# Kernel tuning notes

Hardware: AMD Instinct MI355X
Metric: run time of the kernel (lower is better)

The kernel has to match this reference:

```python
import jax, jax.numpy as jnp
import numpy as np

B, H, W = 16, 64, 64
MODES = 16          # fno_modes (undefined constant in source; standard choice)
HID = 12            # FNO hidden_channels
LIFT = 256          # neuralop default lifting/projection channel width
OUT_CH = 640
N_LAYERS = 4
EPS = 1e-5


def setup_inputs() -> dict:
    key = jax.random.key(0)
    ks = iter(jax.random.split(key, 40))
    r = lambda shape, s=0.05: jax.random.normal(next(ks), shape, dtype=jnp.float32) * s
    inp = {
        "x": jax.random.normal(next(ks), (B, 1, H, W), dtype=jnp.float32),
        "condition": jax.random.normal(next(ks), (B, 2), dtype=jnp.float32),
        # BatchNorm affine params
        "bn2_g": jnp.ones((1,), jnp.float32), "bn2_b": jnp.zeros((1,), jnp.float32),
        "bn1_g": jnp.ones((2,), jnp.float32), "bn1_b": jnp.zeros((2,), jnp.float32),
        # Branch_net: 2 -> 50 -> 50 -> 1, tanh after each
        "b_w1": r((2, 50), 0.5), "b_b1": jnp.zeros((50,), jnp.float32),
        "b_w2": r((50, 50), 0.2), "b_b2": jnp.zeros((50,), jnp.float32),
        "b_w3": r((50, 1), 0.2), "b_b3": jnp.zeros((1,), jnp.float32),
        # FNO lifting MLP: 1 -> 256 -> 12 (1x1 convs)
        "l1_w": r((1, LIFT), 0.5), "l1_b": jnp.zeros((LIFT,), jnp.float32),
        "l2_w": r((LIFT, HID), 0.1), "l2_b": jnp.zeros((HID,), jnp.float32),
        # Spectral conv complex weights (stored real/imag), per layer:
        # block1 = low positive freqs, block2 = negative freqs along axis -2
        "sw1r": r((N_LAYERS, HID, HID, MODES, MODES)),
        "sw1i": r((N_LAYERS, HID, HID, MODES, MODES)),
        "sw2r": r((N_LAYERS, HID, HID, MODES, MODES)),
        "sw2i": r((N_LAYERS, HID, HID, MODES, MODES)),
        # per-layer linear (1x1 conv) skip
        "sk_w": r((N_LAYERS, HID, HID), 0.2),
        "sk_b": jnp.zeros((N_LAYERS, HID), jnp.float32),
        # projection MLP: 12 -> 256 -> 640
        "p1_w": r((HID, LIFT), 0.2), "p1_b": jnp.zeros((LIFT,), jnp.float32),
        "p2_w": r((LIFT, OUT_CH), 0.1), "p2_b": jnp.zeros((OUT_CH,), jnp.float32),
    }
    return inp


def _forward(x, condition, bn2_g, bn2_b, bn1_g, bn1_b,
             b_w1, b_b1, b_w2, b_b2, b_w3, b_b3,
             l1_w, l1_b, l2_w, l2_b,
             sw1r, sw1i, sw2r, sw2i, sk_w, sk_b,
             p1_w, p1_b, p2_w, p2_b):
    gelu = lambda v: jax.nn.gelu(v, approximate=False)

    # BatchNorm2d(1), training-mode batch stats over (B, H, W)
    m = jnp.mean(x, axis=(0, 2, 3), keepdims=True)
    v = jnp.var(x, axis=(0, 2, 3), keepdims=True)
    x_n = (x - m) * jax.lax.rsqrt(v + EPS) * bn2_g[None, :, None, None] + bn2_b[None, :, None, None]

    # BatchNorm1d(2) over batch
    cm = jnp.mean(condition, axis=0, keepdims=True)
    cv = jnp.var(condition, axis=0, keepdims=True)
    c_n = (condition - cm) * jax.lax.rsqrt(cv + EPS) * bn1_g + bn1_b

    # Branch MLP with tanh activations -> [B, 1]
    h = jnp.tanh(c_n @ b_w1 + b_b1)
    h = jnp.tanh(h @ b_w2 + b_b2)
    branch = jnp.tanh(h @ b_w3 + b_b3)

    # FNO lifting: 1x1 conv MLP  [B,1,H,W] -> [B,HID,H,W]
    t = gelu(jnp.einsum('bchw,cd->bdhw', x_n, l1_w) + l1_b[None, :, None, None])
    t = jnp.einsum('bdhw,de->behw', t, l2_w) + l2_b[None, :, None, None]

    Mo = MODES
    for i in range(N_LAYERS):
        xft = jnp.fft.rfft2(t)                          # [B,HID,H,W//2+1] complex
        w1 = sw1r[i] + 1j * sw1i[i]
        w2 = sw2r[i] + 1j * sw2i[i]
        top = jnp.einsum('bchw,cohw->bohw', xft[:, :, :Mo, :Mo], w1)
        bot = jnp.einsum('bchw,cohw->bohw', xft[:, :, -Mo:, :Mo], w2)
        out_ft = jnp.zeros((B, HID, H, W // 2 + 1), dtype=xft.dtype)
        out_ft = out_ft.at[:, :, :Mo, :Mo].set(top).at[:, :, -Mo:, :Mo].set(bot)
        spec = jnp.fft.irfft2(out_ft, s=(H, W))
        skip = jnp.einsum('bchw,co->bohw', t, sk_w[i]) + sk_b[i][None, :, None, None]
        t = spec + skip
        if i < N_LAYERS - 1:
            t = gelu(t)

    # projection: [B,HID,H,W] -> [B,640,H,W]
    q = gelu(jnp.einsum('bchw,cd->bdhw', t, p1_w) + p1_b[None, :, None, None])
    fno_out = jnp.einsum('bdhw,de->behw', q, p2_w) + p2_b[None, :, None, None]

    final = fno_out * branch[:, :, None, None]          # broadcast [B,1,1,1]
    return jnp.transpose(final, (0, 2, 1, 3))           # [B, H, 640, W]


def reference(x, condition, bn2_g, bn2_b, bn1_g, bn1_b,
              b_w1, b_b1, b_w2, b_b2, b_w3, b_b3,
              l1_w, l1_b, l2_w, l2_b,
              sw1r, sw1i, sw2r, sw2i, sk_w, sk_b,
              p1_w, p1_b, p2_w, p2_b):
    return _forward(x, condition, bn2_g, bn2_b, bn1_g, bn1_b,
                    b_w1, b_b1, b_w2, b_b2, b_w3, b_b3,
                    l1_w, l1_b, l2_w, l2_b,
                    sw1r, sw1i, sw2r, sw2i, sk_w, sk_b,
                    p1_w, p1_b, p2_w, p2_b)
```

## Files before the change

### kernel.cpp

```cpp
#include <hip/hip_runtime.h>
#include <math.h>

#define BB 16
#define PIX 4096
#define NPIX 65536
#define HID 12
#define LIFT 256
#define OUT_CH 640
#define EPS 1e-5f

typedef _Float16 half8 __attribute__((ext_vector_type(8)));
typedef float floatx16 __attribute__((ext_vector_type(16)));

__device__ __forceinline__ float gelu_f(float x) {
    return 0.5f * x * (1.0f + erff(x * 0.70710678118654752f));
}

__global__ __launch_bounds__(256) void k_bn_stats(const float* __restrict__ x,
                                                  float* __restrict__ stats) {
    __shared__ float s1[256], s2[256];
    float a = 0.f, b = 0.f;
    for (int i = threadIdx.x; i < NPIX; i += 256) { float v = x[i]; a += v; b += v * v; }
    s1[threadIdx.x] = a; s2[threadIdx.x] = b;
    __syncthreads();
    for (int off = 128; off > 0; off >>= 1) {
        if (threadIdx.x < off) { s1[threadIdx.x] += s1[threadIdx.x + off];
                                 s2[threadIdx.x] += s2[threadIdx.x + off]; }
        __syncthreads();
    }
    if (threadIdx.x == 0) {
        float m = s1[0] / (float)NPIX;
        float var = s2[0] / (float)NPIX - m * m;
        stats[0] = m;
        stats[1] = rsqrtf(var + EPS);
    }
}

__global__ __launch_bounds__(64) void k_branch(const float* __restrict__ cond,
                                               const float* __restrict__ g1, const float* __restrict__ b1,
                                               const float* __restrict__ w1, const float* __restrict__ bb1,
                                               const float* __restrict__ w2, const float* __restrict__ bb2,
                                               const float* __restrict__ w3, const float* __restrict__ bb3,
                                               float* __restrict__ br_out) {
    __shared__ float cm[2], cistd[2];
    int t = threadIdx.x;
    if (t < 2) {
        float s = 0.f;
        for (int i = 0; i < 16; i++) s += cond[i * 2 + t];
        float m = s / 16.f;
        float v = 0.f;
        for (int i = 0; i < 16; i++) { float d = cond[i * 2 + t] - m; v += d * d; }
        v /= 16.f;
        cm[t] = m; cistd[t] = rsqrtf(v + EPS);
    }
    __syncthreads();
    if (t < 16) {
        float c0 = (cond[t * 2 + 0] - cm[0]) * cistd[0] * g1[0] + b1[0];
        float c1 = (cond[t * 2 + 1] - cm[1]) * cistd[1] * g1[1] + b1[1];
        float h1[50], h2[50];
        for (int j = 0; j < 50; j++) h1[j] = tanhf(bb1[j] + c0 * w1[j] + c1 * w1[50 + j]);
        for (int j = 0; j < 50; j++) {
            float acc = bb2[j];
            for (int k = 0; k < 50; k++) acc += h1[k] * w2[k * 50 + j];
            h2[j] = tanhf(acc);
        }
        float acc = bb3[0];
        for (int k = 0; k < 50; k++) acc += h2[k] * w3[k];
        br_out[t] = tanhf(acc);
    }
}

__global__ __launch_bounds__(256) void k_lift(const float* __restrict__ x, const float* __restrict__ stats,
                                              const float* __restrict__ g2, const float* __restrict__ b2,
                                              const float* __restrict__ l1w, const float* __restrict__ l1b,
                                              const float* __restrict__ l2w, const float* __restrict__ l2b,
                                              float* __restrict__ t0) {
    int p = blockIdx.x * 256 + threadIdx.x;
    float m = stats[0], istd = stats[1];
    float xn = (x[p] - m) * istd * g2[0] + b2[0];
    float acc[HID];
#pragma unroll
    for (int e = 0; e < HID; e++) acc[e] = l2b[e];
    for (int d = 0; d < LIFT; d++) {
        float g = gelu_f(xn * l1w[d] + l1b[d]);
#pragma unroll
        for (int e = 0; e < HID; e++) acc[e] += g * l2w[d * HID + e];
    }
    int b = p >> 12, px = p & 4095;
#pragma unroll
    for (int e = 0; e < HID; e++) t0[(b * HID + e) * PIX + px] = acc[e];
}

__global__ __launch_bounds__(256) void k_fwd_w(const float* __restrict__ tin, float2* __restrict__ A) {
    __shared__ float tl[64 * 65];
    __shared__ float ct[64], st[64];
    int bc = blockIdx.x;
    int tid = threadIdx.x;
    if (tid < 64) { float s, c; sincospif(tid * (1.0f / 32.0f), &s, &c); ct[tid] = c; st[tid] = s; }
    const float* src = tin + bc * PIX;
    for (int i = tid; i < PIX; i += 256) {
        int h = i >> 6, w = i & 63;
        tl[h * 65 + w] = src[i];
    }
    __syncthreads();
    for (int o = tid; o < 1024; o += 256) {
        int kw = o >> 6, h = o & 63;
        float xr = 0.f, xi = 0.f;
        for (int w = 0; w < 64; w++) {
            int j = (kw * w) & 63;
            float v = tl[h * 65 + w];
            xr += v * ct[j];
            xi -= v * st[j];
        }
        A[(bc * 16 + kw) * 64 + h] = make_float2(xr, xi);
    }
}

__global__ __launch_bounds__(384) void k_fwd_h_mul(const float2* __restrict__ A,
                                                   const float* __restrict__ w1r, const float* __restrict__ w1i,
                                                   const float* __restrict__ w2r, const float* __restrict__ w2i,
                                                   float2* __restrict__ O) {
    __shared__ float2 Al[12 * 64];
    __shared__ float2 Xl[12 * 32];
    __shared__ float ct[64], st[64];
    int b = blockIdx.x >> 4;
    int kw = blockIdx.x & 15;
    int tid = threadIdx.x;
    if (tid < 64) { float s, c; sincospif(tid * (1.0f / 32.0f), &s, &c); ct[tid] = c; st[tid] = s; }
    for (int i = tid; i < 12 * 64; i += 384) {
        int c = i >> 6, h = i & 63;
        Al[i] = A[((b * 12 + c) * 16 + kw) * 64 + h];
    }
    __syncthreads();
    {
        int c = tid >> 5, kh = tid & 31;
        int f = (kh < 16) ? kh : kh + 32;
        float xr = 0.f, xi = 0.f;
        for (int h = 0; h < 64; h++) {
            int j = (f * h) & 63;
            float2 a = Al[c * 64 + h];
            float cc = ct[j], ss = st[j];
            xr += a.x * cc + a.y * ss;
            xi += a.y * cc - a.x * ss;
        }
        Xl[c * 32 + kh] = make_float2(xr, xi);
    }
    __syncthreads();
    {
        int o = tid >> 5, kh = tid & 31;
        int khr = kh & 15;
        const float* wr = (kh < 16) ? w1r : w2r;
        const float* wi = (kh < 16) ? w1i : w2i;
        float orr = 0.f, oii = 0.f;
        for (int c = 0; c < 12; c++) {
            float2 xv = Xl[c * 32 + kh];
            int wIdx = ((c * 12 + o) * 16 + khr) * 16 + kw;
            float wrv = wr[wIdx], wiv = wi[wIdx];
            orr += xv.x * wrv - xv.y * wiv;
            oii += xv.x * wiv + xv.y * wrv;
        }
        O[((b * 12 + o) * 32 + kh) * 16 + kw] = make_float2(orr, oii);
    }
}

__global__ __launch_bounds__(256) void k_inv(const float2* __restrict__ O, float* __restrict__ spec) {
    __shared__ float2 Ol[32 * 16];
    __shared__ float2 Yl[64 * 17];
    __shared__ float ct[64], st[64];
    int bo = blockIdx.x;
    int tid = threadIdx.x;
    if (tid < 64) { float s, c; sincospif(tid * (1.0f / 32.0f), &s, &c); ct[tid] = c; st[tid] = s; }
    for (int i = tid; i < 512; i += 256) Ol[i] = O[bo * 512 + i];
    __syncthreads();
    for (int oidx = tid; oidx < 1024; oidx += 256) {
        int kw = oidx >> 6, h = oidx & 63;
        float yr = 0.f, yi = 0.f;
        for (int kh = 0; kh < 32; kh++) {
            int f = (kh < 16) ? kh : kh + 32;
            int j = (f * h) & 63;
            float2 ov = Ol[kh * 16 + kw];
            float cc = ct[j], ss = st[j];
            yr += ov.x * cc - ov.y * ss;
            yi += ov.x * ss + ov.y * cc;
        }
        Yl[h * 17 + kw] = make_float2(yr * (1.0f / 4096.0f), yi * (1.0f / 4096.0f));
    }
    __syncthreads();
    for (int i = tid; i < PIX; i += 256) {
        int h = i >> 6, w = i & 63;
        float acc = 0.f;
#pragma unroll
        for (int kw = 0; kw < 16; kw++) {
            int j = (kw * w) & 63;
            float2 yv = Yl[h * 17 + kw];
            float term = yv.x * ct[j] - yv.y * st[j];
            acc += (kw == 0) ? term : 2.0f * term;
        }
        spec[bo * PIX + i] = acc;
    }
}

__global__ __launch_bounds__(256) void k_skip(const float* __restrict__ tin, const float* __restrict__ spec,
                                              const float* __restrict__ skw, const float* __restrict__ skb,
                                              float* __restrict__ tout, int apply_gelu) {
    int p = blockIdx.x * 256 + threadIdx.x;
    int b = p >> 12, px = p & 4095;
    float tr[12];
#pragma unroll
    for (int c = 0; c < 12; c++) tr[c] = tin[(b * 12 + c) * PIX + px];
#pragma unroll
    for (int o = 0; o < 12; o++) {
        float v = spec[(b * 12 + o) * PIX + px] + skb[o];
#pragma unroll
        for (int c = 0; c < 12; c++) v += tr[c] * skw[c * 12 + o];
        if (apply_gelu) v = gelu_f(v);
        tout[(b * 12 + o) * PIX + px] = v;
    }
}

__global__ __launch_bounds__(256) void k_wt(const float* __restrict__ p2w, _Float16* __restrict__ wt) {
    int eg = blockIdx.x;
    int tid = threadIdx.x;
    for (int idx = tid; idx < 1024; idx += 256) {
        int m = idx & 31, kh = (idx >> 5) & 1, ks = idx >> 6;
        half8 v;
#pragma unroll
        for (int j = 0; j < 8; j++)
            v[j] = (_Float16)p2w[(ks * 16 + kh * 8 + j) * 640 + eg * 32 + m];
        *(half8*)&wt[eg * 8192 + ks * 512 + kh * 256 + m * 8] = v;
    }
}

__global__ __launch_bounds__(256, 2) void k_proj_mfma(const float* __restrict__ t,
                                                      const float* __restrict__ p1w,
                                                      const float* __restrict__ p1b,
                                                      const _Float16* __restrict__ wt,
                                                      const float* __restrict__ p2b,
                                                      const float* __restrict__ brn,
                                                      float* __restrict__ out) {
    __shared__ __align__(16) _Float16 ql[128 * 256];
    int pxb = blockIdx.x * 128;
    int eb  = blockIdx.y * 128;
    int tid = threadIdx.x;

    {
        int pxl = tid & 127;
        int dg  = tid >> 7;
        int px  = pxb + pxl;
        int b = px >> 12, pimg = px & 4095;
        float tv[12];
#pragma unroll
        for (int c = 0; c < 12; c++) tv[c] = t[(b * 12 + c) * PIX + pimg];
        int pg = pxl >> 5, pm = pxl & 31;
        for (int dd = 0; dd < 128; dd += 8) {
            half8 hv;
#pragma unroll
            for (int i = 0; i < 8; i++) {
                int d = dg * 128 + dd + i;
                float a = p1b[d];
#pragma unroll
                for (int c = 0; c < 12; c++) a += tv[c] * p1w[c * 256 + d];
                hv[i] = (_Float16)gelu_f(a);
            }
            int d0 = dg * 128 + dd;
            int ks = d0 >> 4, kh = (d0 >> 3) & 1;
            *(half8*)&ql[pg * 8192 + ks * 512 + kh * 256 + pm * 8] = hv;
        }
    }
    __syncthreads();

    int wave = tid >> 6, lane = tid & 63;
    int we = wave >> 1, wp = wave & 1;
    int lo = (lane >> 5) * 256 + (lane & 31) * 8;
    int eg0 = (eb + we * 64) >> 5;
    int pg0 = wp * 2;

    floatx16 acc[2][2];
#pragma unroll
    for (int a = 0; a < 2; a++)
#pragma unroll
        for (int b2 = 0; b2 < 2; b2++)
#pragma unroll
            for (int i = 0; i < 16; i++) acc[a][b2][i] = 0.f;

#pragma unroll
    for (int ks = 0; ks < 16; ks++) {
        half8 a0 = *(const half8*)(wt + eg0 * 8192 + ks * 512 + lo);
        half8 a1 = *(const half8*)(wt + (eg0 + 1) * 8192 + ks * 512 + lo);
        half8 b0 = *(const half8*)&ql[pg0 * 8192 + ks * 512 + lo];
        half8 b1 = *(const half8*)&ql[(pg0 + 1) * 8192 + ks * 512 + lo];
        acc[0][0] = __builtin_amdgcn_mfma_f32_32x32x16_f16(a0, b0, acc[0][0], 0, 0, 0);
        acc[0][1] = __builtin_amdgcn_mfma_f32_32x32x16_f16(a0, b1, acc[0][1], 0, 0, 0);
        acc[1][0] = __builtin_amdgcn_mfma_f32_32x32x16_f16(a1, b0, acc[1][0], 0, 0, 0);
        acc[1][1] = __builtin_amdgcn_mfma_f32_32x32x16_f16(a1, b1, acc[1][1], 0, 0, 0);
    }

    float brv = brn[pxb >> 12];
#pragma unroll
    for (int ta = 0; ta < 2; ta++) {
#pragma unroll
        for (int tb = 0; tb < 2; tb++) {
            int e_base = eb + we * 64 + ta * 32;
            int px = pxb + wp * 64 + tb * 32 + (lane & 31);
            int bh = px >> 6, w = px & 63;
            float* op = out + bh * 640 * 64 + w;
#pragma unroll
            for (int r = 0; r < 16; r++) {
                int row = (r & 3) + 8 * (r >> 2) + 4 * (lane >> 5);
                int e = e_base + row;
                op[e * 64] = (acc[ta][tb][r] + p2b[e]) * brv;
            }
        }
    }
}

extern "C" void kernel_launch(void* const* d_in, const int* in_sizes, int n_in,
                              void* d_out, int out_size, void* d_ws, size_t ws_size,
                              hipStream_t stream) {
    const float* x     = (const float*)d_in[0];
    const float* cond  = (const float*)d_in[1];
    const float* bn2_g = (const float*)d_in[2];
    const float* bn2_b = (const float*)d_in[3];
    const float* bn1_g = (const float*)d_in[4];
    const float* bn1_b = (const float*)d_in[5];
    const float* b_w1  = (const float*)d_in[6];
    const float* b_b1  = (const float*)d_in[7];
    const float* b_w2  = (const float*)d_in[8];
    const float* b_b2  = (const float*)d_in[9];
    const float* b_w3  = (const float*)d_in[10];
    const float* b_b3  = (const float*)d_in[11];
    const float* l1w   = (const float*)d_in[12];
    const float* l1b   = (const float*)d_in[13];
    const float* l2w   = (const float*)d_in[14];
    const float* l2b   = (const float*)d_in[15];
    const float* sw1r  = (const float*)d_in[16];
    const float* sw1i  = (const float*)d_in[17];
    const float* sw2r  = (const float*)d_in[18];
    const float* sw2i  = (const float*)d_in[19];
    const float* skw   = (const float*)d_in[20];
    const float* skb   = (const float*)d_in[21];
    const float* p1w   = (const float*)d_in[22];
    const float* p1b   = (const float*)d_in[23];
    const float* p2w   = (const float*)d_in[24];
    const float* p2b   = (const float*)d_in[25];

    float* ws = (float*)d_ws;
    float* stats = ws;
    float* brn   = ws + 2;
    float* t0    = ws + 32;
    float* t1    = t0 + 786432;
    float2* A    = (float2*)(t1 + 786432);
    float2* O    = A + 196608;
    float* spec  = (float*)(O + 98304);
    _Float16* wt = (_Float16*)(spec + 786432);

    k_bn_stats<<<1, 256, 0, stream>>>(x, stats);
    k_branch<<<1, 64, 0, stream>>>(cond, bn1_g, bn1_b, b_w1, b_b1, b_w2, b_b2, b_w3, b_b3, brn);
    k_lift<<<256, 256, 0, stream>>>(x, stats, bn2_g, bn2_b, l1w, l1b, l2w, l2b, t0);
    k_wt<<<20, 256, 0, stream>>>(p2w, wt);

    float* tin = t0;
    float* tout = t1;
    for (int l = 0; l < 4; l++) {
        k_fwd_w<<<192, 256, 0, stream>>>(tin, A);
        k_fwd_h_mul<<<256, 384, 0, stream>>>(A, sw1r + l * 36864, sw1i + l * 36864,
                                             sw2r + l * 36864, sw2i + l * 36864, O);
        k_inv<<<192, 256, 0, stream>>>(O, spec);
        k_skip<<<256, 256, 0, stream>>>(tin, spec, skw + l * 144, skb + l * 12, tout,
                                        (l < 3) ? 1 : 0);
        float* tmp = tin; tin = tout; tout = tmp;
    }

    k_proj_mfma<<<dim3(512, 5), 256, 0, stream>>>(tin, p1w, p1b, wt, p2b, brn, (float*)d_out);
}
```

Measured before the change: 810.9 us.

## Fuse pre-projection stages into one persistent kernel with grid barriers

```diff
diff --git a/kernel.cpp b/kernel.cpp
--- a/kernel.cpp
+++ b/kernel.cpp
@@ -1,13 +1,10 @@
 #include <hip/hip_runtime.h>
 #include <math.h>
 
-#define BB 16
 #define PIX 4096
 #define NPIX 65536
-#define HID 12
-#define LIFT 256
-#define OUT_CH 640
 #define EPS 1e-5f
+#define NBLK 256u
 
 typedef _Float16 half8 __attribute__((ext_vector_type(8)));
 typedef float floatx16 __attribute__((ext_vector_type(16)));
@@ -16,99 +13,41 @@
     return 0.5f * x * (1.0f + erff(x * 0.70710678118654752f));
 }
 
-__global__ __launch_bounds__(256) void k_bn_stats(const float* __restrict__ x,
-                                                  float* __restrict__ stats) {
-    __shared__ float s1[256], s2[256];
-    float a = 0.f, b = 0.f;
-    for (int i = threadIdx.x; i < NPIX; i += 256) { float v = x[i]; a += v; b += v * v; }
-    s1[threadIdx.x] = a; s2[threadIdx.x] = b;
+__device__ __forceinline__ void gbar(unsigned* cnt) {
+    __threadfence();
     __syncthreads();
-    for (int off = 128; off > 0; off >>= 1) {
-        if (threadIdx.x < off) { s1[threadIdx.x] += s1[threadIdx.x + off];
-                                 s2[threadIdx.x] += s2[threadIdx.x + off]; }
-        __syncthreads();
-    }
     if (threadIdx.x == 0) {
-        float m = s1[0] / (float)NPIX;
-        float var = s2[0] / (float)NPIX - m * m;
-        stats[0] = m;
-        stats[1] = rsqrtf(var + EPS);
-    }
-}
-
-__global__ __launch_bounds__(64) void k_branch(const float* __restrict__ cond,
-                                               const float* __restrict__ g1, const float* __restrict__ b1,
-                                               const float* __restrict__ w1, const float* __restrict__ bb1,
-                                               const float* __restrict__ w2, const float* __restrict__ bb2,
-                                               const float* __restrict__ w3, const float* __restrict__ bb3,
-                                               float* __restrict__ br_out) {
-    __shared__ float cm[2], cistd[2];
-    int t = threadIdx.x;
-    if (t < 2) {
-        float s = 0.f;
-        for (int i = 0; i < 16; i++) s += cond[i * 2 + t];
-        float m = s / 16.f;
-        float v = 0.f;
-        for (int i = 0; i < 16; i++) { float d = cond[i * 2 + t] - m; v += d * d; }
-        v /= 16.f;
-        cm[t] = m; cistd[t] = rsqrtf(v + EPS);
+        __hip_atomic_fetch_add(cnt, 1u, __ATOMIC_ACQ_REL, __HIP_MEMORY_SCOPE_AGENT);
+        while (__hip_atomic_load(cnt, __ATOMIC_ACQUIRE, __HIP_MEMORY_SCOPE_AGENT) < NBLK) {
+            __builtin_amdgcn_s_sleep(1);
+        }
     }
     __syncthreads();
-    if (t < 16) {
-        float c0 = (cond[t * 2 + 0] - cm[0]) * cistd[0] * g1[0] + b1[0];
-        float c1 = (cond[t * 2 + 1] - cm[1]) * cistd[1] * g1[1] + b1[1];
-        float h1[50], h2[50];
-        for (int j = 0; j < 50; j++) h1[j] = tanhf(bb1[j] + c0 * w1[j] + c1 * w1[50 + j]);
-        for (int j = 0; j < 50; j++) {
-            float acc = bb2[j];
-            for (int k = 0; k < 50; k++) acc += h1[k] * w2[k * 50 + j];
-            h2[j] = tanhf(acc);
-        }
-        float acc = bb3[0];
-        for (int k = 0; k < 50; k++) acc += h2[k] * w3[k];
-        br_out[t] = tanhf(acc);
-    }
-}
-
-__global__ __launch_bounds__(256) void k_lift(const float* __restrict__ x, const float* __restrict__ stats,
-                                              const float* __restrict__ g2, const float* __restrict__ b2,
-                                              const float* __restrict__ l1w, const float* __restrict__ l1b,
-                                              const float* __restrict__ l2w, const float* __restrict__ l2b,
-                                              float* __restrict__ t0) {
-    int p = blockIdx.x * 256 + threadIdx.x;
-    float m = stats[0], istd = stats[1];
-    float xn = (x[p] - m) * istd * g2[0] + b2[0];
-    float acc[HID];
-#pragma unroll
-    for (int e = 0; e < HID; e++) acc[e] = l2b[e];
-    for (int d = 0; d < LIFT; d++) {
-        float g = gelu_f(xn * l1w[d] + l1b[d]);
-#pragma unroll
-        for (int e = 0; e < HID; e++) acc[e] += g * l2w[d * HID + e];
-    }
-    int b = p >> 12, px = p & 4095;
-#pragma unroll
-    for (int e = 0; e < HID; e++) t0[(b * HID + e) * PIX + px] = acc[e];
-}
-
-__global__ __launch_bounds__(256) void k_fwd_w(const float* __restrict__ tin, float2* __restrict__ A) {
-    __shared__ float tl[64 * 65];
-    __shared__ float ct[64], st[64];
-    int bc = blockIdx.x;
-    int tid = threadIdx.x;
-    if (tid < 64) { float s, c; sincospif(tid * (1.0f / 32.0f), &s, &c); ct[tid] = c; st[tid] = s; }
-    const float* src = tin + bc * PIX;
-    for (int i = tid; i < PIX; i += 256) {
-        int h = i >> 6, w = i & 63;
-        tl[h * 65 + w] = src[i];
-    }
-    __syncthreads();
+    __threadfence();
+}
+
+struct FusedArgs {
+    const float *x, *cond;
+    const float *bn2_g, *bn2_b, *bn1_g, *bn1_b;
+    const float *b_w1, *b_b1, *b_w2, *b_b2, *b_w3, *b_b3;
+    const float *l1w, *l1b, *l2w, *l2b;
+    const float *sw1r, *sw1i, *sw2r, *sw2i, *skw, *skb;
+    const float *p2w;
+    unsigned *bar;
+    float *brn, *t0, *t1;
+    float2 *A, *O;
+    float *spec;
+    _Float16 *wt;
+};
+
+__device__ __forceinline__ void fwd_w_tile(const float* s_tl, const float* ct, const float* st,
+                                           int bc, float2* A, int tid) {
     for (int o = tid; o < 1024; o += 256) {
         int kw = o >> 6, h = o & 63;
         float xr = 0.f, xi = 0.f;
         for (int w = 0; w < 64; w++) {
             int j = (kw * w) & 63;
-            float v = tl[h * 65 + w];
+            float v = s_tl[h * 65 + w];
             xr += v * ct[j];
             xi -= v * st[j];
         }
@@ -116,131 +55,221 @@
     }
 }
 
-__global__ __launch_bounds__(384) void k_fwd_h_mul(const float2* __restrict__ A,
-                                                   const float* __restrict__ w1r, const float* __restrict__ w1i,
-                                                   const float* __restrict__ w2r, const float* __restrict__ w2i,
-                                                   float2* __restrict__ O) {
-    __shared__ float2 Al[12 * 64];
-    __shared__ float2 Xl[12 * 32];
+__global__ __launch_bounds__(256) void k_fused(FusedArgs a) {
+    __shared__ float s_tl[64 * 65];
+    __shared__ float s_aux[3200];
     __shared__ float ct[64], st[64];
-    int b = blockIdx.x >> 4;
-    int kw = blockIdx.x & 15;
-    int tid = threadIdx.x;
+    __shared__ float s_red[512];
+    __shared__ float cms[4];
+    int blk = blockIdx.x, tid = threadIdx.x;
+    int bi = 0;
+
     if (tid < 64) { float s, c; sincospif(tid * (1.0f / 32.0f), &s, &c); ct[tid] = c; st[tid] = s; }
-    for (int i = tid; i < 12 * 64; i += 384) {
-        int c = i >> 6, h = i & 63;
-        Al[i] = A[((b * 12 + c) * 16 + kw) * 64 + h];
-    }
-    __syncthreads();
+
+    float bn_m, bn_istd;
     {
-        int c = tid >> 5, kh = tid & 31;
-        int f = (kh < 16) ? kh : kh + 32;
-        float xr = 0.f, xi = 0.f;
-        for (int h = 0; h < 64; h++) {
-            int j = (f * h) & 63;
-            float2 a = Al[c * 64 + h];
-            float cc = ct[j], ss = st[j];
-            xr += a.x * cc + a.y * ss;
-            xi += a.y * cc - a.x * ss;
-        }
-        Xl[c * 32 + kh] = make_float2(xr, xi);
-    }
-    __syncthreads();
+        float aa = 0.f, bb = 0.f;
+        for (int i = tid; i < NPIX; i += 256) { float v = a.x[i]; aa += v; bb += v * v; }
+        s_red[tid] = aa; s_red[256 + tid] = bb;
+        __syncthreads();
+        for (int off = 128; off > 0; off >>= 1) {
+            if (tid < off) { s_red[tid] += s_red[tid + off]; s_red[256 + tid] += s_red[256 + tid + off]; }
+            __syncthreads();
+        }
+        bn_m = s_red[0] * (1.0f / NPIX);
+        float var = s_red[256] * (1.0f / NPIX) - bn_m * bn_m;
+        bn_istd = rsqrtf(var + EPS);
+    }
+
+    if (blk < 20) {
+        int eg = blk;
+        for (int idx = tid; idx < 1024; idx += 256) {
+            int m = idx & 31, kh = (idx >> 5) & 1, ks = idx >> 6;
+            half8 v;
+#pragma unroll
+            for (int j = 0; j < 8; j++)
+                v[j] = (_Float16)a.p2w[(ks * 16 + kh * 8 + j) * 640 + eg * 32 + m];
+            *(half8*)&a.wt[eg * 8192 + ks * 512 + kh * 256 + m * 8] = v;
+        }
+    }
+
+    if (blk == 255) {
+        if (tid < 2) {
+            float s = 0.f;
+            for (int i = 0; i < 16; i++) s += a.cond[i * 2 + tid];
+            float m = s / 16.f, v = 0.f;
+            for (int i = 0; i < 16; i++) { float d = a.cond[i * 2 + tid] - m; v += d * d; }
+            cms[tid] = m; cms[2 + tid] = rsqrtf(v / 16.f + EPS);
+        }
+        __syncthreads();
+        if (tid < 16) {
+            float c0 = (a.cond[tid * 2 + 0] - cms[0]) * cms[2] * a.bn1_g[0] + a.bn1_b[0];
+            float c1 = (a.cond[tid * 2 + 1] - cms[1]) * cms[3] * a.bn1_g[1] + a.bn1_b[1];
+            float h1[50], h2[50];
+            for (int j = 0; j < 50; j++) h1[j] = tanhf(a.b_b1[j] + c0 * a.b_w1[j] + c1 * a.b_w1[50 + j]);
+            for (int j = 0; j < 50; j++) {
+                float acc = a.b_b2[j];
+                for (int k = 0; k < 50; k++) acc += h1[k] * a.b_w2[k * 50 + j];
+                h2[j] = tanhf(acc);
+            }
+            float acc = a.b_b3[0];
+            for (int k = 0; k < 50; k++) acc += h2[k] * a.b_w3[k];
+            a.brn[tid] = tanhf(acc);
+        }
+    }
+
     {
-        int o = tid >> 5, kh = tid & 31;
-        int khr = kh & 15;
-        const float* wr = (kh < 16) ? w1r : w2r;
-        const float* wi = (kh < 16) ? w1i : w2i;
-        float orr = 0.f, oii = 0.f;
-        for (int c = 0; c < 12; c++) {
-            float2 xv = Xl[c * 32 + kh];
-            int wIdx = ((c * 12 + o) * 16 + khr) * 16 + kw;
-            float wrv = wr[wIdx], wiv = wi[wIdx];
-            orr += xv.x * wrv - xv.y * wiv;
-            oii += xv.x * wiv + xv.y * wrv;
-        }
-        O[((b * 12 + o) * 32 + kh) * 16 + kw] = make_float2(orr, oii);
-    }
-}
-
-__global__ __launch_bounds__(256) void k_inv(const float2* __restrict__ O, float* __restrict__ spec) {
-    __shared__ float2 Ol[32 * 16];
-    __shared__ float2 Yl[64 * 17];
-    __shared__ float ct[64], st[64];
-    int bo = blockIdx.x;
-    int tid = threadIdx.x;
-    if (tid < 64) { float s, c; sincospif(tid * (1.0f / 32.0f), &s, &c); ct[tid] = c; st[tid] = s; }
-    for (int i = tid; i < 512; i += 256) Ol[i] = O[bo * 512 + i];
-    __syncthreads();
-    for (int oidx = tid; oidx < 1024; oidx += 256) {
-        int kw = oidx >> 6, h = oidx & 63;
-        float yr = 0.f, yi = 0.f;
-        for (int kh = 0; kh < 32; kh++) {
-            int f = (kh < 16) ? kh : kh + 32;
-            int j = (f * h) & 63;
-            float2 ov = Ol[kh * 16 + kw];
-            float cc = ct[j], ss = st[j];
-            yr += ov.x * cc - ov.y * ss;
-            yi += ov.x * ss + ov.y * cc;
-        }
-        Yl[h * 17 + kw] = make_float2(yr * (1.0f / 4096.0f), yi * (1.0f / 4096.0f));
-    }
-    __syncthreads();
-    for (int i = tid; i < PIX; i += 256) {
-        int h = i >> 6, w = i & 63;
-        float acc = 0.f;
-#pragma unroll
-        for (int kw = 0; kw < 16; kw++) {
-            int j = (kw * w) & 63;
-            float2 yv = Yl[h * 17 + kw];
-            float term = yv.x * ct[j] - yv.y * st[j];
-            acc += (kw == 0) ? term : 2.0f * term;
-        }
-        spec[bo * PIX + i] = acc;
-    }
-}
-
-__global__ __launch_bounds__(256) void k_skip(const float* __restrict__ tin, const float* __restrict__ spec,
-                                              const float* __restrict__ skw, const float* __restrict__ skb,
-                                              float* __restrict__ tout, int apply_gelu) {
-    int p = blockIdx.x * 256 + threadIdx.x;
-    int b = p >> 12, px = p & 4095;
-    float tr[12];
-#pragma unroll
-    for (int c = 0; c < 12; c++) tr[c] = tin[(b * 12 + c) * PIX + px];
-#pragma unroll
-    for (int o = 0; o < 12; o++) {
-        float v = spec[(b * 12 + o) * PIX + px] + skb[o];
-#pragma unroll
-        for (int c = 0; c < 12; c++) v += tr[c] * skw[c * 12 + o];
-        if (apply_gelu) v = gelu_f(v);
-        tout[(b * 12 + o) * PIX + px] = v;
-    }
-}
-
-__global__ __launch_bounds__(256) void k_wt(const float* __restrict__ p2w, _Float16* __restrict__ wt) {
-    int eg = blockIdx.x;
-    int tid = threadIdx.x;
-    for (int idx = tid; idx < 1024; idx += 256) {
-        int m = idx & 31, kh = (idx >> 5) & 1, ks = idx >> 6;
-        half8 v;
-#pragma unroll
-        for (int j = 0; j < 8; j++)
-            v[j] = (_Float16)p2w[(ks * 16 + kh * 8 + j) * 640 + eg * 32 + m];
-        *(half8*)&wt[eg * 8192 + ks * 512 + kh * 256 + m * 8] = v;
-    }
-}
-
-__global__ __launch_bounds__(256, 2) void k_proj_mfma(const float* __restrict__ t,
-                                                      const float* __restrict__ p1w,
-                                                      const float* __restrict__ p1b,
-                                                      const _Float16* __restrict__ wt,
-                                                      const float* __restrict__ p2b,
-                                                      const float* __restrict__ brn,
-                                                      float* __restrict__ out) {
+        int p = blk * 256 + tid;
+        float xn = (a.x[p] - bn_m) * bn_istd * a.bn2_g[0] + a.bn2_b[0];
+        float acc[12];
+#pragma unroll
+        for (int e = 0; e < 12; e++) acc[e] = a.l2b[e];
+        for (int d = 0; d < 256; d++) {
+            float g = gelu_f(xn * a.l1w[d] + a.l1b[d]);
+#pragma unroll
+            for (int e = 0; e < 12; e++) acc[e] += g * a.l2w[d * 12 + e];
+        }
+        int b = p >> 12, px = p & 4095;
+#pragma unroll
+        for (int e = 0; e < 12; e++) a.t0[(b * 12 + e) * PIX + px] = acc[e];
+    }
+    gbar(&a.bar[bi++]);
+
+    const float* tin = a.t0;
+    float* tout = a.t1;
+
+    if (blk < 192) {
+        for (int i = tid; i < PIX; i += 256) s_tl[(i >> 6) * 65 + (i & 63)] = tin[blk * PIX + i];
+        __syncthreads();
+        fwd_w_tile(s_tl, ct, st, blk, a.A, tid);
+    }
+    gbar(&a.bar[bi++]);
+
+    for (int l = 0; l < 4; l++) {
+        const float* w1r = a.sw1r + l * 36864; const float* w1i = a.sw1i + l * 36864;
+        const float* w2r = a.sw2r + l * 36864; const float* w2i = a.sw2i + l * 36864;
+
+        {
+            int b = blk >> 4, kw = blk & 15;
+            float2* Al = (float2*)s_aux;
+            float2* Xl = (float2*)(s_aux + 1536);
+            for (int i = tid; i < 768; i += 256) {
+                int c = i >> 6, h = i & 63;
+                Al[i] = a.A[((b * 12 + c) * 16 + kw) * 64 + h];
+            }
+            __syncthreads();
+            for (int o = tid; o < 384; o += 256) {
+                int c = o >> 5, kh = o & 31;
+                int f = (kh < 16) ? kh : kh + 32;
+                float xr = 0.f, xi = 0.f;
+                for (int h = 0; h < 64; h++) {
+                    int j = (f * h) & 63;
+                    float2 av = Al[c * 64 + h];
+                    float cc = ct[j], ss = st[j];
+                    xr += av.x * cc + av.y * ss;
+                    xi += av.y * cc - av.x * ss;
+                }
+                Xl[c * 32 + kh] = make_float2(xr, xi);
+            }
+            __syncthreads();
+            for (int o2 = tid; o2 < 384; o2 += 256) {
+                int o = o2 >> 5, kh = o2 & 31;
+                int khr = kh & 15;
+                const float* wr = (kh < 16) ? w1r : w2r;
+                const float* wi = (kh < 16) ? w1i : w2i;
+                float orr = 0.f, oii = 0.f;
+                for (int c = 0; c < 12; c++) {
+                    float2 xv = Xl[c * 32 + kh];
+                    int wIdx = ((c * 12 + o) * 16 + khr) * 16 + kw;
+                    float wrv = wr[wIdx], wiv = wi[wIdx];
+                    orr += xv.x * wrv - xv.y * wiv;
+                    oii += xv.x * wiv + xv.y * wrv;
+                }
+                a.O[((b * 12 + o) * 32 + kh) * 16 + kw] = make_float2(orr, oii);
+            }
+        }
+        gbar(&a.bar[bi++]);
+
+        if (blk < 192) {
+            int b = blk / 12, oc = blk % 12;
+            float2* Ol = (float2*)s_aux;
+            float2* Yl = (float2*)(s_aux + 1024);
+            for (int i = tid; i < 512; i += 256) Ol[i] = a.O[blk * 512 + i];
+            __syncthreads();
+            for (int oidx = tid; oidx < 1024; oidx += 256) {
+                int kw = oidx >> 6, h = oidx & 63;
+                float yr = 0.f, yi = 0.f;
+                for (int kh = 0; kh < 32; kh++) {
+                    int f = (kh < 16) ? kh : kh + 32;
+                    int j = (f * h) & 63;
+                    float2 ov = Ol[kh * 16 + kw];
+                    float cc = ct[j], ss = st[j];
+                    yr += ov.x * cc - ov.y * ss;
+                    yi += ov.x * ss + ov.y * cc;
+                }
+                Yl[h * 17 + kw] = make_float2(yr * (1.0f / 4096.0f), yi * (1.0f / 4096.0f));
+            }
+            __syncthreads();
+            for (int i = tid; i < PIX; i += 256) {
+                int h = i >> 6, w = i & 63;
+                float acc = 0.f;
+#pragma unroll
+                for (int kw = 0; kw < 16; kw++) {
+                    int j = (kw * w) & 63;
+                    float2 yv = Yl[h * 17 + kw];
+                    float term = yv.x * ct[j] - yv.y * st[j];
+                    acc += (kw == 0) ? term : 2.0f * term;
+                }
+                s_tl[h * 65 + w] = acc;
+            }
+            __syncthreads();
+            if (l < 3) {
+                for (int i = tid; i < PIX; i += 256) {
+                    int h = i >> 6, w = i & 63;
+                    float v = s_tl[h * 65 + w] + a.skb[l * 12 + oc];
+                    for (int c = 0; c < 12; c++)
+                        v += tin[(b * 12 + c) * PIX + i] * a.skw[l * 144 + c * 12 + oc];
+                    v = gelu_f(v);
+                    s_tl[h * 65 + w] = v;
+                    tout[(b * 12 + oc) * PIX + i] = v;
+                }
+                __syncthreads();
+                fwd_w_tile(s_tl, ct, st, blk, a.A, tid);
+            } else {
+                for (int i = tid; i < PIX; i += 256)
+                    a.spec[blk * PIX + i] = s_tl[(i >> 6) * 65 + (i & 63)];
+            }
+        }
+        gbar(&a.bar[bi++]);
+
+        if (l < 3) { const float* tmp = tin; tin = tout; tout = (float*)tmp; }
+    }
+
+    {
+        int p = blk * 256 + tid;
+        int b = p >> 12, px = p & 4095;
+        float tr[12];
+#pragma unroll
+        for (int c = 0; c < 12; c++) tr[c] = tin[(b * 12 + c) * PIX + px];
+#pragma unroll
+        for (int o = 0; o < 12; o++) {
+            float v = a.spec[(b * 12 + o) * PIX + px] + a.skb[36 + o];
+#pragma unroll
+            for (int c = 0; c < 12; c++) v += tr[c] * a.skw[432 + c * 12 + o];
+            tout[(b * 12 + o) * PIX + px] = v;
+        }
+    }
+}
+
+__global__ __launch_bounds__(256, 2) void k_proj2(const float* __restrict__ t,
+                                                  const float* __restrict__ p1w,
+                                                  const float* __restrict__ p1b,
+                                                  const _Float16* __restrict__ wt,
+                                                  const float* __restrict__ p2b,
+                                                  const float* __restrict__ brn,
+                                                  float* __restrict__ out) {
     __shared__ __align__(16) _Float16 ql[128 * 256];
     int pxb = blockIdx.x * 128;
-    int eb  = blockIdx.y * 128;
     int tid = threadIdx.x;
 
     {
@@ -257,10 +286,10 @@
 #pragma unroll
             for (int i = 0; i < 8; i++) {
                 int d = dg * 128 + dd + i;
-                float a = p1b[d];
-#pragma unroll
-                for (int c = 0; c < 12; c++) a += tv[c] * p1w[c * 256 + d];
-                hv[i] = (_Float16)gelu_f(a);
+                float aa = p1b[d];
+#pragma unroll
+                for (int c = 0; c < 12; c++) aa += tv[c] * p1w[c * 256 + d];
+                hv[i] = (_Float16)gelu_f(aa);
             }
             int d0 = dg * 128 + dd;
             int ks = d0 >> 4, kh = (d0 >> 3) & 1;
@@ -272,43 +301,47 @@
     int wave = tid >> 6, lane = tid & 63;
     int we = wave >> 1, wp = wave & 1;
     int lo = (lane >> 5) * 256 + (lane & 31) * 8;
-    int eg0 = (eb + we * 64) >> 5;
     int pg0 = wp * 2;
-
-    floatx16 acc[2][2];
-#pragma unroll
-    for (int a = 0; a < 2; a++)
-#pragma unroll
-        for (int b2 = 0; b2 < 2; b2++)
-#pragma unroll
-            for (int i = 0; i < 16; i++) acc[a][b2][i] = 0.f;
-
-#pragma unroll
-    for (int ks = 0; ks < 16; ks++) {
-        half8 a0 = *(const half8*)(wt + eg0 * 8192 + ks * 512 + lo);
-        half8 a1 = *(const half8*)(wt + (eg0 + 1) * 8192 + ks * 512 + lo);
-        half8 b0 = *(const half8*)&ql[pg0 * 8192 + ks * 512 + lo];
-        half8 b1 = *(const half8*)&ql[(pg0 + 1) * 8192 + ks * 512 + lo];
-        acc[0][0] = __builtin_amdgcn_mfma_f32_32x32x16_f16(a0, b0, acc[0][0], 0, 0, 0);
-        acc[0][1] = __builtin_amdgcn_mfma_f32_32x32x16_f16(a0, b1, acc[0][1], 0, 0, 0);
-        acc[1][0] = __builtin_amdgcn_mfma_f32_32x32x16_f16(a1, b0, acc[1][0], 0, 0, 0);
-        acc[1][1] = __builtin_amdgcn_mfma_f32_32x32x16_f16(a1, b1, acc[1][1], 0, 0, 0);
-    }
-
     float brv = brn[pxb >> 12];
-#pragma unroll
-    for (int ta = 0; ta < 2; ta++) {
-#pragma unroll
-        for (int tb = 0; tb < 2; tb++) {
-            int e_base = eb + we * 64 + ta * 32;
-            int px = pxb + wp * 64 + tb * 32 + (lane & 31);
-            int bh = px >> 6, w = px & 63;
-            float* op = out + bh * 640 * 64 + w;
-#pragma unroll
-            for (int r = 0; r < 16; r++) {
-                int row = (r & 3) + 8 * (r >> 2) + 4 * (lane >> 5);
-                int e = e_base + row;
-                op[e * 64] = (acc[ta][tb][r] + p2b[e]) * brv;
+
+    for (int ebi = 0; ebi < 5; ebi++) {
+        int eb = ebi * 128;
+        int eg0 = (eb + we * 64) >> 5;
+
+        floatx16 acc[2][2];
+#pragma unroll
+        for (int aa = 0; aa < 2; aa++)
+#pragma unroll
+            for (int b2 = 0; b2 < 2; b2++)
+#pragma unroll
+                for (int i = 0; i < 16; i++) acc[aa][b2][i] = 0.f;
+
+#pragma unroll
+        for (int ks = 0; ks < 16; ks++) {
+            half8 a0 = *(const half8*)(wt + eg0 * 8192 + ks * 512 + lo);
+            half8 a1 = *(const half8*)(wt + (eg0 + 1) * 8192 + ks * 512 + lo);
+            half8 b0 = *(const half8*)&ql[pg0 * 8192 + ks * 512 + lo];
+            half8 b1 = *(const half8*)&ql[(pg0 + 1) * 8192 + ks * 512 + lo];
+            acc[0][0] = __builtin_amdgcn_mfma_f32_32x32x16_f16(a0, b0, acc[0][0], 0, 0, 0);
+            acc[0][1] = __builtin_amdgcn_mfma_f32_32x32x16_f16(a0, b1, acc[0][1], 0, 0, 0);
+            acc[1][0] = __builtin_amdgcn_mfma_f32_32x32x16_f16(a1, b0, acc[1][0], 0, 0, 0);
+            acc[1][1] = __builtin_amdgcn_mfma_f32_32x32x16_f16(a1, b1, acc[1][1], 0, 0, 0);
+        }
+
+#pragma unroll
+        for (int ta = 0; ta < 2; ta++) {
+#pragma unroll
+            for (int tb = 0; tb < 2; tb++) {
+                int e_base = eb + we * 64 + ta * 32;
+                int px = pxb + wp * 64 + tb * 32 + (lane & 31);
+                int bh = px >> 6, w = px & 63;
+                float* op = out + bh * 640 * 64 + w;
+#pragma unroll
+                for (int r = 0; r < 16; r++) {
+                    int row = (r & 3) + 8 * (r >> 2) + 4 * (lane >> 5);
+                    int e = e_base + row;
+                    op[e * 64] = (acc[ta][tb][r] + p2b[e]) * brv;
+                }
             }
         }
     }
@@ -317,59 +350,38 @@
 extern "C" void kernel_launch(void* const* d_in, const int* in_sizes, int n_in,
                               void* d_out, int out_size, void* d_ws, size_t ws_size,
                               hipStream_t stream) {
-    const float* x     = (const float*)d_in[0];
-    const float* cond  = (const float*)d_in[1];
-    const float* bn2_g = (const float*)d_in[2];
-    const float* bn2_b = (const float*)d_in[3];
-    const float* bn1_g = (const float*)d_in[4];
-    const float* bn1_b = (const float*)d_in[5];
-    const float* b_w1  = (const float*)d_in[6];
-    const float* b_b1  = (const float*)d_in[7];
-    const float* b_w2  = (const float*)d_in[8];
-    const float* b_b2  = (const float*)d_in[9];
-    const float* b_w3  = (const float*)d_in[10];
-    const float* b_b3  = (const float*)d_in[11];
-    const float* l1w   = (const float*)d_in[12];
-    const float* l1b   = (const float*)d_in[13];
-    const float* l2w   = (const float*)d_in[14];
-    const float* l2b   = (const float*)d_in[15];
-    const float* sw1r  = (const float*)d_in[16];
-    const float* sw1i  = (const float*)d_in[17];
-    const float* sw2r  = (const float*)d_in[18];
-    const float* sw2i  = (const float*)d_in[19];
-    const float* skw   = (const float*)d_in[20];
-    const float* skb   = (const float*)d_in[21];
-    const float* p1w   = (const float*)d_in[22];
-    const float* p1b   = (const float*)d_in[23];
-    const float* p2w   = (const float*)d_in[24];
-    const float* p2b   = (const float*)d_in[25];
-
     float* ws = (float*)d_ws;
-    float* stats = ws;
-    float* brn   = ws + 2;
-    float* t0    = ws + 32;
-    float* t1    = t0 + 786432;
-    float2* A    = (float2*)(t1 + 786432);
-    float2* O    = A + 196608;
-    float* spec  = (float*)(O + 98304);
+    unsigned* bar = (unsigned*)ws;
+    float* brn  = ws + 16;
+    float* t0   = ws + 32;
+    float* t1   = t0 + 786432;
+    float2* A   = (float2*)(t1 + 786432);
+    float2* O   = A + 196608;
+    float* spec = (float*)(O + 98304);
     _Float16* wt = (_Float16*)(spec + 786432);
 
-    k_bn_stats<<<1, 256, 0, stream>>>(x, stats);
-    k_branch<<<1, 64, 0, stream>>>(cond, bn1_g, bn1_b, b_w1, b_b1, b_w2, b_b2, b_w3, b_b3, brn);
-    k_lift<<<256, 256, 0, stream>>>(x, stats, bn2_g, bn2_b, l1w, l1b, l2w, l2b, t0);
-    k_wt<<<20, 256, 0, stream>>>(p2w, wt);
-
-    float* tin = t0;
-    float* tout = t1;
-    for (int l = 0; l < 4; l++) {
-        k_fwd_w<<<192, 256, 0, stream>>>(tin, A);
-        k_fwd_h_mul<<<256, 384, 0, stream>>>(A, sw1r + l * 36864, sw1i + l * 36864,
-                                             sw2r + l * 36864, sw2i + l * 36864, O);
-        k_inv<<<192, 256, 0, stream>>>(O, spec);
-        k_skip<<<256, 256, 0, stream>>>(tin, spec, skw + l * 144, skb + l * 12, tout,
-                                        (l < 3) ? 1 : 0);
-        float* tmp = tin; tin = tout; tout = tmp;
-    }
-
-    k_proj_mfma<<<dim3(512, 5), 256, 0, stream>>>(tin, p1w, p1b, wt, p2b, brn, (float*)d_out);
-}
+    hipMemsetAsync(bar, 0, 64, stream);
+
+    FusedArgs fa;
+    fa.x = (const float*)d_in[0];   fa.cond = (const float*)d_in[1];
+    fa.bn2_g = (const float*)d_in[2]; fa.bn2_b = (const float*)d_in[3];
+    fa.bn1_g = (const float*)d_in[4]; fa.bn1_b = (const float*)d_in[5];
+    fa.b_w1 = (const float*)d_in[6];  fa.b_b1 = (const float*)d_in[7];
+    fa.b_w2 = (const float*)d_in[8];  fa.b_b2 = (const float*)d_in[9];
+    fa.b_w3 = (const float*)d_in[10]; fa.b_b3 = (const float*)d_in[11];
+    fa.l1w = (const float*)d_in[12];  fa.l1b = (const float*)d_in[13];
+    fa.l2w = (const float*)d_in[14];  fa.l2b = (const float*)d_in[15];
+    fa.sw1r = (const float*)d_in[16]; fa.sw1i = (const float*)d_in[17];
+    fa.sw2r = (const float*)d_in[18]; fa.sw2i = (const float*)d_in[19];
+    fa.skw = (const float*)d_in[20];  fa.skb = (const float*)d_in[21];
+    fa.p2w = (const float*)d_in[24];
+    fa.bar = bar;
+    fa.brn = brn; fa.t0 = t0; fa.t1 = t1; fa.A = A; fa.O = O; fa.spec = spec; fa.wt = wt;
+
+    k_fused<<<256, 256, 0, stream>>>(fa);
+
+    const float* p1w = (const float*)d_in[22];
+    const float* p1b = (const float*)d_in[23];
+    const float* p2b = (const float*)d_in[25];
+    k_proj2<<<512, 256, 0, stream>>>(t0, p1w, p1b, wt, p2b, brn, (float*)d_out);
+}
```

After: 1.181 ms. 45.7% more time.
